# Kernel tuning notes

Measured on AMD Instinct MI355X. Metric: run time of the kernel, lower is better.

The kernel has to match this reference:

```python
import jax, jax.numpy as jnp
import numpy as np

C = 1.0                     # curvature
BALL_EPS = 1e-3             # pmath.project boundary epsilon (float32)
ATANH_CLAMP = 1.0 - 1e-5    # artanh argument clamp
MIN_DENOM = 1e-15
INIT_NORM = 0.4             # prototype_init_norm


def setup_inputs() -> dict:
    key = jax.random.key(0)
    kx, kr, kp = jax.random.split(key, 3)
    N, K, D = 16384, 128, 64
    # Points strictly inside the Poincare ball: random direction * radius in [0, 0.8)
    v = jax.random.normal(kx, (N, D), dtype=jnp.float32)
    v = v / jnp.maximum(jnp.linalg.norm(v, axis=-1, keepdims=True), 1e-8)
    r = jax.random.uniform(kr, (N, 1), dtype=jnp.float32) * 0.8
    x = v * r
    # Prototypes: unit directions scaled to init norm (as in __init__)
    p = jax.random.normal(kp, (K, D), dtype=jnp.float32)
    p = p / jnp.maximum(jnp.linalg.norm(p, axis=-1, keepdims=True), 1e-8)
    prototypes = p * INIT_NORM
    return {"x": x, "prototypes": prototypes}


def _project_ball(p, c):
    # pmath.project: clamp norm to (1 - eps) / sqrt(c)
    maxnorm = (1.0 - BALL_EPS) / jnp.sqrt(c)
    n = jnp.maximum(jnp.linalg.norm(p, axis=-1, keepdims=True), 1e-15)
    return p * jnp.minimum(1.0, maxnorm / n)


def reference(x, prototypes):
    c = jnp.float32(C)
    sqrt_c = jnp.sqrt(c)
    p = _project_ball(prototypes, c)            # (K, D)

    xe = x[:, None, :]                          # (N, 1, D)
    pe = p[None, :, :]                          # (1, K, D)
    x2 = jnp.sum(xe * xe, axis=-1, keepdims=True)   # (N, 1, 1)
    p2 = jnp.sum(pe * pe, axis=-1, keepdims=True)   # (1, K, 1)
    xy = jnp.sum(xe * pe, axis=-1, keepdims=True)   # (N, K, 1)

    # mobius_add(-x, p) with u = -x: <u,p> = -<x,p>, ||u||^2 = ||x||^2
    num = (1.0 - 2.0 * c * xy + c * p2) * (-xe) + (1.0 - c * x2) * pe  # (N,K,D)
    den = 1.0 - 2.0 * c * xy + (c * c) * x2 * p2                       # (N,K,1)
    ma = num / jnp.maximum(den, MIN_DENOM)

    ma_norm = jnp.sqrt(jnp.sum(ma * ma, axis=-1))        # (N, K)
    z = jnp.clip(sqrt_c * ma_norm, 0.0, ATANH_CLAMP)
    dist = (2.0 / sqrt_c) * jnp.arctanh(z)               # geodesic distance
    return -(dist * dist)                                # logits (N, K)
```

## Files before the change

kernel.cpp:

```cpp
#include <hip/hip_runtime.h>
#include <math.h>


#define K_PROTO 128
#define D_DIM   64
#define BN      64
#define STRIDE  68

__global__ __launch_bounds__(256) void geodesic_kernel(
    const float* __restrict__ x,
    const float* __restrict__ p,
    float* __restrict__ out)
{
    __shared__ __align__(16) float xs[BN * STRIDE];
    __shared__ __align__(16) float ps[K_PROTO * STRIDE];
    __shared__ float sx2[BN];
    __shared__ float sp2[K_PROTO];
    __shared__ float ssc[K_PROTO];

    const int t  = threadIdx.x;
    const int n0 = blockIdx.x * BN;

    #pragma unroll
    for (int it = 0; it < 4; ++it) {
        int idx = t + 256 * it;
        int r   = idx >> 4;
        int c4  = (idx & 15) << 2;
        float4 v = *(const float4*)(x + (size_t)(n0 + r) * D_DIM + c4);
        *(float4*)(&xs[r * STRIDE + c4]) = v;
    }
    #pragma unroll
    for (int it = 0; it < 8; ++it) {
        int idx = t + 256 * it;
        int r   = idx >> 4;
        int c4  = (idx & 15) << 2;
        float4 v = *(const float4*)(p + (size_t)r * D_DIM + c4);
        *(float4*)(&ps[r * STRIDE + c4]) = v;
    }
    __syncthreads();

    if (t < K_PROTO) {
        float s2 = 0.f;
        #pragma unroll
        for (int i = 0; i < 16; ++i) {
            float4 v = *(const float4*)(&ps[t * STRIDE + 4 * i]);
            s2 += v.x * v.x + v.y * v.y + v.z * v.z + v.w * v.w;
        }
        float nrm = fmaxf(sqrtf(s2), 1e-15f);
        float sc  = fminf(1.0f, 0.999f / nrm);
        ssc[t] = sc;
        sp2[t] = s2 * sc * sc;
    } else if (t < K_PROTO + BN) {
        int r = t - K_PROTO;
        float s2 = 0.f;
        #pragma unroll
        for (int i = 0; i < 16; ++i) {
            float4 v = *(const float4*)(&xs[r * STRIDE + 4 * i]);
            s2 += v.x * v.x + v.y * v.y + v.z * v.z + v.w * v.w;
        }
        sx2[r] = s2;
    }
    __syncthreads();

    const int tk = t & 15;
    const int tn = t >> 4;

    float acc[4][8];
    #pragma unroll
    for (int a = 0; a < 4; ++a)
        #pragma unroll
        for (int b = 0; b < 8; ++b) acc[a][b] = 0.f;

    #pragma unroll 4
    for (int i = 0; i < 16; ++i) {
        float4 xa[4], pa[8];
        #pragma unroll
        for (int jn = 0; jn < 4; ++jn)
            xa[jn] = *(const float4*)(&xs[(tn + 16 * jn) * STRIDE + 4 * i]);
        #pragma unroll
        for (int jk = 0; jk < 8; ++jk)
            pa[jk] = *(const float4*)(&ps[(tk + 16 * jk) * STRIDE + 4 * i]);
        #pragma unroll
        for (int jn = 0; jn < 4; ++jn)
            #pragma unroll
            for (int jk = 0; jk < 8; ++jk) {
                acc[jn][jk] += xa[jn].x * pa[jk].x + xa[jn].y * pa[jk].y
                             + xa[jn].z * pa[jk].z + xa[jn].w * pa[jk].w;
            }
    }

    float p2v[8], scv[8];
    #pragma unroll
    for (int jk = 0; jk < 8; ++jk) {
        int k = tk + 16 * jk;
        p2v[jk] = sp2[k];
        scv[jk] = ssc[k];
    }

    #pragma unroll
    for (int jn = 0; jn < 4; ++jn) {
        int n = tn + 16 * jn;
        float x2 = sx2[n];
        float b  = 1.0f - x2;
        float* orow = out + (size_t)(n0 + n) * K_PROTO;
        #pragma unroll
        for (int jk = 0; jk < 8; ++jk) {
            float xy  = acc[jn][jk] * scv[jk];
            float p2  = p2v[jk];
            float a   = 1.0f - 2.0f * xy + p2;
            float den = fmaxf(1.0f - 2.0f * xy + x2 * p2, 1e-15f);
            float num2 = fmaxf(a * a * x2 - 2.0f * a * b * xy + b * b * p2, 0.0f);
            float z   = fminf(__fdividef(sqrtf(num2), den), 1.0f - 1e-05f);
            float l   = __logf(__fdividef(1.0f + z, 1.0f - z));
            orow[tk + 16 * jk] = -(l * l);
        }
    }
}

extern "C" void kernel_launch(void* const* d_in, const int* in_sizes, int n_in,
                              void* d_out, int out_size, void* d_ws, size_t ws_size,
                              hipStream_t stream) {
    const float* x = (const float*)d_in[0];
    const float* p = (const float*)d_in[1];
    float* out = (float*)d_out;

    dim3 grid(16384 / BN);
    dim3 block(256);
    hipLaunchKernelGGL(geodesic_kernel, grid, block, 0, stream, x, p, out);
}
```

Before: 68.70 us.

## Shrink row tile to 16 and use one row per thread for more blocks

```diff
diff --git a/kernel.cpp b/kernel.cpp
--- a/kernel.cpp
+++ b/kernel.cpp
@@ -4,16 +4,16 @@
 
 #define K_PROTO 128
 #define D_DIM   64
-#define BN      64
+#define BN      16
 #define STRIDE  68
 
-__global__ __launch_bounds__(256) void geodesic_kernel(
+__global__ __launch_bounds__(256, 4) void geodesic_kernel(
     const float* __restrict__ x,
     const float* __restrict__ p,
     float* __restrict__ out)
 {
+    __shared__ __align__(16) float ps[K_PROTO * STRIDE];
     __shared__ __align__(16) float xs[BN * STRIDE];
-    __shared__ __align__(16) float ps[K_PROTO * STRIDE];
     __shared__ float sx2[BN];
     __shared__ float sp2[K_PROTO];
     __shared__ float ssc[K_PROTO];
@@ -21,11 +21,9 @@
     const int t  = threadIdx.x;
     const int n0 = blockIdx.x * BN;
 
-    #pragma unroll
-    for (int it = 0; it < 4; ++it) {
-        int idx = t + 256 * it;
-        int r   = idx >> 4;
-        int c4  = (idx & 15) << 2;
+    {
+        int r  = t >> 4;
+        int c4 = (t & 15) << 2;
         float4 v = *(const float4*)(x + (size_t)(n0 + r) * D_DIM + c4);
         *(float4*)(&xs[r * STRIDE + c4]) = v;
     }
@@ -62,58 +60,38 @@
     }
     __syncthreads();
 
-    const int tk = t & 15;
-    const int tn = t >> 4;
+    const int tn = t & 15;
+    const int kg = t >> 4;
 
-    float acc[4][8];
+    float acc[8];
     #pragma unroll
-    for (int a = 0; a < 4; ++a)
+    for (int m = 0; m < 8; ++m) acc[m] = 0.f;
+
+    #pragma unroll 2
+    for (int i = 0; i < 16; ++i) {
+        float4 xv = *(const float4*)(&xs[tn * STRIDE + 4 * i]);
         #pragma unroll
-        for (int b = 0; b < 8; ++b) acc[a][b] = 0.f;
-
-    #pragma unroll 4
-    for (int i = 0; i < 16; ++i) {
-        float4 xa[4], pa[8];
-        #pragma unroll
-        for (int jn = 0; jn < 4; ++jn)
-            xa[jn] = *(const float4*)(&xs[(tn + 16 * jn) * STRIDE + 4 * i]);
-        #pragma unroll
-        for (int jk = 0; jk < 8; ++jk)
-            pa[jk] = *(const float4*)(&ps[(tk + 16 * jk) * STRIDE + 4 * i]);
-        #pragma unroll
-        for (int jn = 0; jn < 4; ++jn)
-            #pragma unroll
-            for (int jk = 0; jk < 8; ++jk) {
-                acc[jn][jk] += xa[jn].x * pa[jk].x + xa[jn].y * pa[jk].y
-                             + xa[jn].z * pa[jk].z + xa[jn].w * pa[jk].w;
-            }
+        for (int m = 0; m < 8; ++m) {
+            float4 pv = *(const float4*)(&ps[(kg + 16 * m) * STRIDE + 4 * i]);
+            acc[m] += xv.x * pv.x + xv.y * pv.y + xv.z * pv.z + xv.w * pv.w;
+        }
     }
 
-    float p2v[8], scv[8];
-    #pragma unroll
-    for (int jk = 0; jk < 8; ++jk) {
-        int k = tk + 16 * jk;
-        p2v[jk] = sp2[k];
-        scv[jk] = ssc[k];
-    }
+    const float x2 = sx2[tn];
+    const float b  = 1.0f - x2;
+    float* orow = out + (size_t)(n0 + tn) * K_PROTO;
 
     #pragma unroll
-    for (int jn = 0; jn < 4; ++jn) {
-        int n = tn + 16 * jn;
-        float x2 = sx2[n];
-        float b  = 1.0f - x2;
-        float* orow = out + (size_t)(n0 + n) * K_PROTO;
-        #pragma unroll
-        for (int jk = 0; jk < 8; ++jk) {
-            float xy  = acc[jn][jk] * scv[jk];
-            float p2  = p2v[jk];
-            float a   = 1.0f - 2.0f * xy + p2;
-            float den = fmaxf(1.0f - 2.0f * xy + x2 * p2, 1e-15f);
-            float num2 = fmaxf(a * a * x2 - 2.0f * a * b * xy + b * b * p2, 0.0f);
-            float z   = fminf(__fdividef(sqrtf(num2), den), 1.0f - 1e-05f);
-            float l   = __logf(__fdividef(1.0f + z, 1.0f - z));
-            orow[tk + 16 * jk] = -(l * l);
-        }
+    for (int m = 0; m < 8; ++m) {
+        int   k   = kg + 16 * m;
+        float xy  = acc[m] * ssc[k];
+        float p2  = sp2[k];
+        float a   = 1.0f - 2.0f * xy + p2;
+        float den = fmaxf(1.0f - 2.0f * xy + x2 * p2, 1e-15f);
+        float num2 = fmaxf(a * a * x2 - 2.0f * a * b * xy + b * b * p2, 0.0f);
+        float z   = fminf(__fdividef(sqrtf(num2), den), 1.0f - 1e-05f);
+        float l   = __logf(__fdividef(1.0f + z, 1.0f - z));
+        orow[k] = -(l * l);
     }
 }
 
```

Result: no change. 69.41 us (+1.0%).
